# Performance work log

Measured on AMD Instinct MI355X. Metric: run time of the kernel, lower is better.

The kernel has to match this reference:

```python
import jax, jax.numpy as jnp
import numpy as np

DIM = 3
N = DIM * DIM          # 9 digits
NUM_NODES = N * N      # 81 cells
HID = 96
EMB = 16

def sudoku_edges():
    edges = []
    for r in range(N):
        for c in range(N):
            s = set()
            for k in range(N):
                s.add(r * N + k)
                s.add(k * N + c)
            br, bc = (r // DIM) * DIM, (c // DIM) * DIM
            for dr in range(DIM):
                for dc in range(DIM):
                    s.add((br + dr) * N + (bc + dc))
            s.discard(r * N + c)
            edges.append(sorted(s))
    return np.asarray(edges, np.int32)  # (81, 20)

EDGES = jnp.asarray(sudoku_edges())

def mlp(x, params):
    # ReLU between hidden layers, no activation after the last layer
    for w, b in params[:-1]:
        x = jax.nn.relu(x @ w + b)
    w, b = params[-1]
    return x @ w + b

def setup_inputs():
    key = jax.random.key(0)
    ks = iter(jax.random.split(key, 64))
    B = 256
    def p(shape, scale=0.1):
        return jax.random.normal(next(ks), shape, jnp.float32) * scale
    inp = {}
    inp['grids'] = jax.random.randint(next(ks), (B, NUM_NODES), 0, 3)
    inp['iters'] = 8
    inp['emb'] = p((3, EMB))
    inp['in_w0'] = p((EMB, HID)); inp['in_b0'] = jnp.zeros((HID,), jnp.float32)
    inp['in_w1'] = p((HID, HID)); inp['in_b1'] = jnp.zeros((HID,), jnp.float32)
    inp['in_w2'] = p((HID, HID)); inp['in_b2'] = jnp.zeros((HID,), jnp.float32)
    inp['rel_w0'] = p((2 * HID, HID)); inp['rel_b0'] = jnp.zeros((HID,), jnp.float32)
    inp['rel_w1'] = p((HID, HID)); inp['rel_b1'] = jnp.zeros((HID,), jnp.float32)
    inp['rel_w2'] = p((HID, HID)); inp['rel_b2'] = jnp.zeros((HID,), jnp.float32)
    inp['g_w0'] = p((2 * HID, HID)); inp['g_b0'] = jnp.zeros((HID,), jnp.float32)
    inp['g_w1'] = p((HID, HID)); inp['g_b1'] = jnp.zeros((HID,), jnp.float32)
    inp['g_w2'] = p((HID, HID)); inp['g_b2'] = jnp.zeros((HID,), jnp.float32)
    inp['lstm_wih'] = p((HID, 4 * HID)); inp['lstm_whh'] = p((HID, 4 * HID))
    inp['lstm_bih'] = jnp.zeros((4 * HID,), jnp.float32)
    inp['lstm_bhh'] = jnp.zeros((4 * HID,), jnp.float32)
    inp['r_w0'] = p((HID, HID)); inp['r_b0'] = jnp.zeros((HID,), jnp.float32)
    inp['r_w1'] = p((HID, HID)); inp['r_b1'] = jnp.zeros((HID,), jnp.float32)
    inp['r_w2'] = p((HID, N)); inp['r_b2'] = jnp.zeros((N,), jnp.float32)
    inp['c0'] = p((B * NUM_NODES, HID), 1.0)  # torch.randn LSTM cell init
    return inp

def reference(grids, iters, emb, in_w0, in_b0, in_w1, in_b1, in_w2, in_b2,
              rel_w0, rel_b0, rel_w1, rel_b1, rel_w2, rel_b2,
              g_w0, g_b0, g_w1, g_b1, g_w2, g_b2,
              lstm_wih, lstm_whh, lstm_bih, lstm_bhh,
              r_w0, r_b0, r_w1, r_b1, r_w2, r_b2, c0):
    B = grids.shape[0]
    in_p = [(in_w0, in_b0), (in_w1, in_b1), (in_w2, in_b2)]
    rel_p = [(rel_w0, rel_b0), (rel_w1, rel_b1), (rel_w2, rel_b2)]
    g_p = [(g_w0, g_b0), (g_w1, g_b1), (g_w2, g_b2)]
    r_p = [(r_w0, r_b0), (r_w1, r_b1), (r_w2, r_b2)]
    X = mlp(emb[grids], in_p)                     # (B, 81, 96)
    H0 = jax.lax.stop_gradient(X)                 # X.clone().detach()
    h = H0.reshape(B * NUM_NODES, HID)
    bias = lstm_bih + lstm_bhh

    def step(carry, _):
        h, c = carry
        Hn = h.reshape(B, NUM_NODES, HID)
        nbr = Hn[:, EDGES]                        # (B, 81, 20, 96) neighbor gather
        self_f = jnp.broadcast_to(Hn[:, :, None], nbr.shape)
        msgs = mlp(jnp.concatenate([self_f, nbr], axis=-1), rel_p)
        M = msgs.sum(axis=2)                      # scatter-sum of messages
        x_in = mlp(jnp.concatenate([X, M], axis=-1), g_p).reshape(B * NUM_NODES, HID)
        gates = x_in @ lstm_wih + h @ lstm_whh + bias
        i, f, g, o = jnp.split(gates, 4, axis=-1)  # torch gate order i,f,g,o
        c2 = jax.nn.sigmoid(f) * c + jax.nn.sigmoid(i) * jnp.tanh(g)
        h2 = jax.nn.sigmoid(o) * jnp.tanh(c2)
        out = mlp(h2.reshape(B, NUM_NODES, HID), r_p)  # (B, 81, 9)
        return (h2, c2), out

    _, outputs = jax.lax.scan(step, (h, c0), None, length=iters)
    return outputs  # (iters, B, 81, 9)
```

## Files before the change

### kernel.cpp

```cpp
#include <hip/hip_runtime.h>
#include <hip/hip_bf16.h>
#include <stdint.h>

typedef __attribute__((ext_vector_type(8))) short short8v;
typedef __attribute__((ext_vector_type(4))) float float4v;

#define DEVI __device__ __forceinline__

constexpr int BATCH = 256;
constexpr int NN   = 81;
constexpr int HID  = 96;
constexpr int NOUT = 9;
constexpr int BLOCK = 512;
constexpr int LDA = 100;
constexpr int LDB = 104;

constexpr int OFF_XG = 0;
constexpr int OFF_H0 = 7776;
constexpr int OFF_H1 = 11988;
constexpr int OFF_MS = 16200;
constexpr int OFF_AP = 24300;
constexpr int OFF_BV = 32400;
constexpr int SMEM_F = 40500;

constexpr int W_REL0A = 0;
constexpr int W_REL0B = 18432;
constexpr int W_REL1  = 36864;
constexpr int W_REL2  = 55296;
constexpr int W_G0B   = 73728;
constexpr int W_G1    = 92160;
constexpr int W_G2    = 110592;
constexpr int W_IH    = 129024;
constexpr int W_HH    = 202752;
constexpr int W_R0    = 276480;
constexpr int W_R1    = 294912;
constexpr int W_R2    = 313344;
constexpr int W_IN1   = 316416;
constexpr int W_IN2   = 334848;
constexpr int W_G0A   = 353280;

DEVI float sigm(float x)  { return 1.f / (1.f + __expf(-x)); }
DEVI float tanh_(float x) { return 1.f - 2.f / (__expf(2.f * x) + 1.f); }

DEVI short bfhi(float x) { union { float f; unsigned u; } v; v.f = x; return (short)(v.u >> 16); }
DEVI float fromBits(short s) { union { unsigned u; float f; } v; v.u = ((unsigned)(unsigned short)s) << 16; return v.f; }
DEVI short bfrne(float x) {
  union { float f; unsigned u; } v; v.f = x;
  unsigned r = v.u + 0x7fffu + ((v.u >> 16) & 1u);
  return (short)(r >> 16);
}
DEVI void split1(float x, short& h, short& l) { h = bfhi(x); l = bfrne(x - fromBits(h)); }

DEVI void packFrag(const float* p, short8v& v) {
  const float4 a = *reinterpret_cast<const float4*>(p);
  const float4 b = *reinterpret_cast<const float4*>(p + 4);
  v[0] = bfrne(a.x); v[1] = bfrne(a.y); v[2] = bfrne(a.z); v[3] = bfrne(a.w);
  v[4] = bfrne(b.x); v[5] = bfrne(b.y); v[6] = bfrne(b.z); v[7] = bfrne(b.w);
}
DEVI void packFragPair(const float* ap, const float* bp, short8v& v) {
  const float4 a0 = *reinterpret_cast<const float4*>(ap);
  const float4 a1 = *reinterpret_cast<const float4*>(ap + 4);
  const float4 b0 = *reinterpret_cast<const float4*>(bp);
  const float4 b1 = *reinterpret_cast<const float4*>(bp + 4);
  v[0] = bfrne(fmaxf(a0.x + b0.x, 0.f)); v[1] = bfrne(fmaxf(a0.y + b0.y, 0.f));
  v[2] = bfrne(fmaxf(a0.z + b0.z, 0.f)); v[3] = bfrne(fmaxf(a0.w + b0.w, 0.f));
  v[4] = bfrne(fmaxf(a1.x + b1.x, 0.f)); v[5] = bfrne(fmaxf(a1.y + b1.y, 0.f));
  v[6] = bfrne(fmaxf(a1.z + b1.z, 0.f)); v[7] = bfrne(fmaxf(a1.w + b1.w, 0.f));
}

DEVI float4v mfma2(short8v a, short8v bh, short8v bl, float4v acc) {
  acc = __builtin_amdgcn_mfma_f32_16x16x32_bf16(a, bh, acc, 0, 0, 0);
  acc = __builtin_amdgcn_mfma_f32_16x16x32_bf16(a, bl, acc, 0, 0, 0);
  return acc;
}

DEVI int nbr_of(int n, int e) {
  const int r = n / 9, c = n - 9 * r;
  if (e < 8)  { int cc = c + 1 + e;  if (cc >= 9) cc -= 9; return r * 9 + cc; }
  if (e < 16) { int rr = r + e - 7;  if (rr >= 9) rr -= 9; return rr * 9 + c; }
  const int q = e - 16, dr = 1 + (q >> 1), dc = 1 + (q & 1);
  const int rm = r % 3, cm = c % 3;
  int rr = r - rm + rm + dr; rr -= (rm + dr >= 3) ? 3 : 0;
  int cc = c - cm + cm + dc; cc -= (cm + dc >= 3) ? 3 : 0;
  return rr * 9 + cc;
}

__global__ __launch_bounds__(64)
void pack_kernel(const float* rel_w0, const float* rel_w1, const float* rel_w2,
                 const float* g_w0, const float* g_w1, const float* g_w2,
                 const float* wih, const float* whh,
                 const float* r_w0, const float* r_w1, const float* r_w2,
                 const float* in_w1, const float* in_w2, short* ws)
{
  const int lane = threadIdx.x;
  const int blk = blockIdx.x;
  const int starts[16] = {0,18,36,54,72,90,108,126,198,270,288,306,309,327,345,363};
  int mi = 0;
  while (blk >= starts[mi + 1]) ++mi;
  const int tt = blk - starts[mi];
  const int ntile = starts[mi + 1] - starts[mi];
  const float* src; int C = 96, row0 = 0, off;
  switch (mi) {
    case 0:  src = rel_w0; off = W_REL0A; break;
    case 1:  src = rel_w0; row0 = 96; off = W_REL0B; break;
    case 2:  src = rel_w1; off = W_REL1; break;
    case 3:  src = rel_w2; off = W_REL2; break;
    case 4:  src = g_w0; row0 = 96; off = W_G0B; break;
    case 5:  src = g_w1; off = W_G1; break;
    case 6:  src = g_w2; off = W_G2; break;
    case 7:  src = wih; C = 384; off = W_IH; break;
    case 8:  src = whh; C = 384; off = W_HH; break;
    case 9:  src = r_w0; off = W_R0; break;
    case 10: src = r_w1; off = W_R1; break;
    case 11: src = r_w2; C = 9; off = W_R2; break;
    case 12: src = in_w1; off = W_IN1; break;
    case 13: src = in_w2; off = W_IN2; break;
    default: src = g_w0; off = W_G0A; break;
  }
  const int kt = tt % 3, ct = tt / 3;
  const int q = lane >> 4, r = lane & 15;
  const int c = ct * 16 + r;
  short* hd = ws + off + tt * 512 + lane * 8;
  short* ld = hd + ntile * 512;
  #pragma unroll
  for (int j = 0; j < 8; ++j) {
    const int k = row0 + kt * 32 + q * 8 + j;
    float w = (c < C) ? src[k * C + c] : 0.f;
    short h, l; split1(w, h, l);
    hd[j] = h; ld[j] = l;
  }
}

template<bool ABF, bool OBF, bool RELU, bool XGADD>
DEVI void stage96(float* sm, int aOff, const short* WS, int wOff, int wTiles,
                  const float* bias, float bscale, int dOff, int dstLDf,
                  int wave, int lane)
{
  const int rl = lane & 15, q = lane >> 4;
  const int plane = wTiles * 512;
  const short* asb = reinterpret_cast<const short*>(sm + aOff);
  short* dsb = reinterpret_cast<short*>(sm + dOff);
  float* dsf = sm + dOff;
  #pragma unroll 1
  for (int t = wave; t < 18; t += 8) {
    const int rtp = t % 3, ct = t / 3;
    short8v a2[2][3];
    #pragma unroll
    for (int sub = 0; sub < 2; ++sub) {
      const int row = rtp * 32 + sub * 16 + rl;
      if (ABF) {
        const short* ap = asb + row * LDB + q * 8;
        #pragma unroll
        for (int kt = 0; kt < 3; ++kt)
          a2[sub][kt] = *reinterpret_cast<const short8v*>(ap + kt * 32);
      } else {
        const float* ap = &sm[aOff + row * LDA + q * 8];
        #pragma unroll
        for (int kt = 0; kt < 3; ++kt) packFrag(ap + kt * 32, a2[sub][kt]);
      }
    }
    float4v acc0 = {0.f, 0.f, 0.f, 0.f}, acc1 = {0.f, 0.f, 0.f, 0.f};
    #pragma unroll
    for (int kt = 0; kt < 3; ++kt) {
      const short* bp = WS + wOff + (ct * 3 + kt) * 512 + lane * 8;
      const short8v bh = *reinterpret_cast<const short8v*>(bp);
      const short8v bl = *reinterpret_cast<const short8v*>(bp + plane);
      acc0 = mfma2(a2[0][kt], bh, bl, acc0);
      acc1 = mfma2(a2[1][kt], bh, bl, acc1);
    }
    const int col = ct * 16 + rl;
    #pragma unroll
    for (int sub = 0; sub < 2; ++sub) {
      #pragma unroll
      for (int j = 0; j < 4; ++j) {
        const int row = rtp * 32 + sub * 16 + q * 4 + j;
        if (row < NN) {
          float v = sub ? acc1[j] : acc0[j];
          if (bias)  v += bias[col] * bscale;
          if (XGADD) v += sm[OFF_XG + row * 96 + col];
          if (RELU)  v = fmaxf(v, 0.f);
          if (OBF) dsb[row * LDB + col] = bfrne(v);
          else     dsf[row * dstLDf + col] = v;
        }
      }
    }
  }
}

__global__ __launch_bounds__(BLOCK) __attribute__((amdgpu_waves_per_eu(1, 2)))
void rrn_kernel(const int* __restrict__ grids, const int* __restrict__ itersp,
                const float* __restrict__ emb, const float* __restrict__ in_w0,
                const float* __restrict__ in_b0, const float* __restrict__ in_b1,
                const float* __restrict__ in_b2,
                const float* __restrict__ rel_b0, const float* __restrict__ rel_b1,
                const float* __restrict__ rel_b2,
                const float* __restrict__ g_b0, const float* __restrict__ g_b1,
                const float* __restrict__ g_b2,
                const float* __restrict__ bih, const float* __restrict__ bhh,
                const float* __restrict__ r_b0, const float* __restrict__ r_b1,
                const float* __restrict__ r_b2,
                const float* __restrict__ c0, const short* __restrict__ WS,
                float* __restrict__ out)
{
  __shared__ float sm[SMEM_F];
  const int b = blockIdx.x, tid = threadIdx.x;
  const int wave = tid >> 6, lane = tid & 63;
  const int rl = lane & 15, q = lane >> 4;
  const int iters = itersp[0];

  float creg[6][4];
  #pragma unroll
  for (int rt = 0; rt < 6; ++rt)
    #pragma unroll
    for (int j = 0; j < 4; ++j) creg[rt][j] = 0.f;
  if (wave < 6) {
    #pragma unroll
    for (int rt = 0; rt < 6; ++rt) {
      #pragma unroll
      for (int j = 0; j < 4; ++j) {
        const int n = rt * 16 + q * 4 + j, col = wave * 16 + rl;
        creg[rt][j] = (n < NN) ? c0[(size_t)b * NN * HID + n * HID + col] : 0.f;
      }
    }
  }

  for (int t = tid; t < NN * HID; t += BLOCK) {
    const int n = t / HID, col = t - n * HID;
    const int g = grids[b * NN + n];
    float acc = in_b0[col];
    #pragma unroll
    for (int k = 0; k < 16; ++k) acc += emb[g * 16 + k] * in_w0[k * HID + col];
    sm[OFF_AP + n * LDA + col] = fmaxf(acc, 0.f);
  }
  __syncthreads();
  stage96<false, true, true,  false>(sm, OFF_AP, WS, W_IN1, 18, in_b1, 1.f, OFF_MS, 0, wave, lane);
  __syncthreads();
  stage96<true,  true, false, false>(sm, OFF_MS, WS, W_IN2, 18, in_b2, 1.f, OFF_H0, 0, wave, lane);
  __syncthreads();
  stage96<true, false, false, false>(sm, OFF_H0, WS, W_G0A, 18, g_b0,  1.f, OFF_XG, 96, wave, lane);
  __syncthreads();

  for (int it = 0; it < iters; ++it) {
    const int hc = (it & 1) ? OFF_H1 : OFF_H0;
    const int hn = (it & 1) ? OFF_H0 : OFF_H1;

    for (int i = tid; i < 8100; i += BLOCK) sm[OFF_MS + i] = 0.f;
    stage96<true, false, false, false>(sm, hc, WS, W_REL0A, 18, rel_b0, 1.f, OFF_AP, LDA, wave, lane);
    stage96<true, false, false, false>(sm, hc, WS, W_REL0B, 18, nullptr, 0.f, OFF_BV, LDA, wave, lane);
    __syncthreads();

    #pragma unroll 1
    for (int g2 = wave; g2 < 51; g2 += 8) {
      short8v a2[2][3];
      #pragma unroll
      for (int sub = 0; sub < 2; ++sub) {
        const int row = g2 * 32 + sub * 16 + rl;
        if (row < 1620) {
          const int n = row / 20, e = row - 20 * n, m = nbr_of(n, e);
          const float* ap = &sm[OFF_AP + n * LDA + q * 8];
          const float* bp = &sm[OFF_BV + m * LDA + q * 8];
          #pragma unroll
          for (int kt = 0; kt < 3; ++kt)
            packFragPair(ap + kt * 32, bp + kt * 32, a2[sub][kt]);
        } else {
          const short8v z = {0,0,0,0,0,0,0,0};
          #pragma unroll
          for (int kt = 0; kt < 3; ++kt) a2[sub][kt] = z;
        }
      }
      #pragma unroll 1
      for (int ct = 0; ct < 6; ++ct) {
        const float rb1c = rel_b1[ct * 16 + rl];
        float4v acc0 = {0,0,0,0}, acc1 = {0,0,0,0};
        #pragma unroll
        for (int kt = 0; kt < 3; ++kt) {
          const short* bp = WS + W_REL1 + (ct * 3 + kt) * 512 + lane * 8;
          const short8v bh = *reinterpret_cast<const short8v*>(bp);
          const short8v bl = *reinterpret_cast<const short8v*>(bp + 18 * 512);
          acc0 = mfma2(a2[0][kt], bh, bl, acc0);
          acc1 = mfma2(a2[1][kt], bh, bl, acc1);
        }
        const int col = ct * 16 + rl;
        #pragma unroll
        for (int sub = 0; sub < 2; ++sub) {
          const int r0 = g2 * 32 + sub * 16 + q * 4;
          if (r0 < 1620) {
            const int node = r0 / 20;
            const float4v a = sub ? acc1 : acc0;
            const float s = fmaxf(a[0] + rb1c, 0.f) + fmaxf(a[1] + rb1c, 0.f)
                          + fmaxf(a[2] + rb1c, 0.f) + fmaxf(a[3] + rb1c, 0.f);
            atomicAdd(&sm[OFF_MS + node * LDA + col], s);
          }
        }
        __builtin_amdgcn_sched_barrier(0);
      }
    }
    __syncthreads();

    stage96<false, true, false, false>(sm, OFF_MS, WS, W_REL2, 18, rel_b2, 20.f, OFF_AP, 0, wave, lane);
    __syncthreads();
    stage96<true, true, true, true >(sm, OFF_AP, WS, W_G0B, 18, nullptr, 0.f, OFF_MS, 0, wave, lane);
    __syncthreads();
    stage96<true, true, true, false>(sm, OFF_MS, WS, W_G1, 18, g_b1, 1.f, OFF_AP, 0, wave, lane);
    __syncthreads();
    stage96<true, true, false, false>(sm, OFF_AP, WS, W_G2, 18, g_b2, 1.f, OFF_MS, 0, wave, lane);
    __syncthreads();

    if (wave < 6) {
      const int colh = wave * 16 + rl;
      const short* xs = reinterpret_cast<const short*>(sm + OFF_MS);
      const short* hs = reinterpret_cast<const short*>(sm + hc);
      short* hnp = reinterpret_cast<short*>(sm + hn);
      #pragma unroll
      for (int rt = 0; rt < 6; ++rt) {
        const int row = rt * 16 + rl;
        short8v af[6];
        #pragma unroll
        for (int kt = 0; kt < 3; ++kt)
          af[kt] = *reinterpret_cast<const short8v*>(xs + row * LDB + kt * 32 + q * 8);
        #pragma unroll
        for (int kt = 3; kt < 6; ++kt)
          af[kt] = *reinterpret_cast<const short8v*>(hs + row * LDB + (kt - 3) * 32 + q * 8);
        float4v ga[4];
        #pragma unroll
        for (int gate = 0; gate < 4; ++gate) {
          const int ct = gate * 6 + wave;
          float4v acc = {0.f, 0.f, 0.f, 0.f};
          #pragma unroll
          for (int kt = 0; kt < 3; ++kt) {
            const short* bp = WS + W_IH + (ct * 3 + kt) * 512 + lane * 8;
            acc = mfma2(af[kt], *reinterpret_cast<const short8v*>(bp),
                        *reinterpret_cast<const short8v*>(bp + 72 * 512), acc);
          }
          __builtin_amdgcn_sched_barrier(0);
          #pragma unroll
          for (int kt = 3; kt < 6; ++kt) {
            const short* bp = WS + W_HH + (ct * 3 + kt - 3) * 512 + lane * 8;
            acc = mfma2(af[kt], *reinterpret_cast<const short8v*>(bp),
                        *reinterpret_cast<const short8v*>(bp + 72 * 512), acc);
          }
          ga[gate] = acc;
          __builtin_amdgcn_sched_barrier(0);
        }
        #pragma unroll
        for (int j = 0; j < 4; ++j) {
          const int n = rt * 16 + q * 4 + j;
          const float gi = ga[0][j] + bih[colh]       + bhh[colh];
          const float gf = ga[1][j] + bih[96 + colh]  + bhh[96 + colh];
          const float gg = ga[2][j] + bih[192 + colh] + bhh[192 + colh];
          const float go = ga[3][j] + bih[288 + colh] + bhh[288 + colh];
          const float c2 = sigm(gf) * creg[rt][j] + sigm(gi) * tanh_(gg);
          creg[rt][j] = c2;
          if (n < NN) hnp[n * LDB + colh] = bfrne(sigm(go) * tanh_(c2));
        }
      }
    }
    __syncthreads();

    stage96<true, true, true, false>(sm, hn, WS, W_R0, 18, r_b0, 1.f, OFF_AP, 0, wave, lane);
    __syncthreads();
    stage96<true, true, true, false>(sm, OFF_AP, WS, W_R1, 18, r_b1, 1.f, OFF_MS, 0, wave, lane);
    __syncthreads();
    if (wave < 3) {
      const int rtp = wave;
      const short* asb = reinterpret_cast<const short*>(sm + OFF_MS);
      short8v a2[2][3];
      #pragma unroll
      for (int sub = 0; sub < 2; ++sub) {
        const int row = rtp * 32 + sub * 16 + rl;
        #pragma unroll
        for (int kt = 0; kt < 3; ++kt)
          a2[sub][kt] = *reinterpret_cast<const short8v*>(asb + row * LDB + kt * 32 + q * 8);
      }
      float4v a0 = {0,0,0,0}, a1 = {0,0,0,0};
      #pragma unroll
      for (int kt = 0; kt < 3; ++kt) {
        const short* bp = WS + W_R2 + kt * 512 + lane * 8;
        const short8v bh = *reinterpret_cast<const short8v*>(bp);
        const short8v bl = *reinterpret_cast<const short8v*>(bp + 3 * 512);
        a0 = mfma2(a2[0][kt], bh, bl, a0);
        a1 = mfma2(a2[1][kt], bh, bl, a1);
      }
      if (rl < NOUT) {
        float* op = out + ((size_t)it * BATCH + b) * NN * NOUT;
        #pragma unroll
        for (int sub = 0; sub < 2; ++sub)
          #pragma unroll
          for (int j = 0; j < 4; ++j) {
            const int row = rtp * 32 + sub * 16 + q * 4 + j;
            if (row < NN) op[row * NOUT + rl] = (sub ? a1[j] : a0[j]) + r_b2[rl];
          }
      }
    }
    __syncthreads();
  }
}

extern "C" void kernel_launch(void* const* d_in, const int* in_sizes, int n_in,
                              void* d_out, int out_size, void* d_ws, size_t ws_size,
                              hipStream_t stream) {
  (void)in_sizes; (void)n_in; (void)out_size; (void)ws_size;
  const int* grids = (const int*)d_in[0];
  const int* iters = (const int*)d_in[1];
  const float *emb = (const float*)d_in[2],
    *in_w0 = (const float*)d_in[3],  *in_b0 = (const float*)d_in[4],
    *in_b1 = (const float*)d_in[6],  *in_b2 = (const float*)d_in[8],
    *rel_w0 = (const float*)d_in[9],  *rel_b0 = (const float*)d_in[10],
    *rel_w1 = (const float*)d_in[11], *rel_b1 = (const float*)d_in[12],
    *rel_w2 = (const float*)d_in[13], *rel_b2 = (const float*)d_in[14],
    *g_w0 = (const float*)d_in[15], *g_b0 = (const float*)d_in[16],
    *g_w1 = (const float*)d_in[17], *g_b1 = (const float*)d_in[18],
    *g_w2 = (const float*)d_in[19], *g_b2 = (const float*)d_in[20],
    *wih = (const float*)d_in[21], *whh = (const float*)d_in[22],
    *bih = (const float*)d_in[23], *bhh = (const float*)d_in[24],
    *r_w0 = (const float*)d_in[25], *r_b0 = (const float*)d_in[26],
    *r_w1 = (const float*)d_in[27], *r_b1 = (const float*)d_in[28],
    *r_w2 = (const float*)d_in[29], *r_b2 = (const float*)d_in[30],
    *c0 = (const float*)d_in[31];
  short* ws = (short*)d_ws;
  pack_kernel<<<dim3(363), dim3(64), 0, stream>>>(
      rel_w0, rel_w1, rel_w2, g_w0, g_w1, g_w2, wih, whh,
      r_w0, r_w1, r_w2, (const float*)d_in[5], (const float*)d_in[7], ws);
  rrn_kernel<<<dim3(BATCH), dim3(BLOCK), 0, stream>>>(
      grids, iters, emb, in_w0, in_b0, in_b1, in_b2,
      rel_b0, rel_b1, rel_b2, g_b0, g_b1, g_b2,
      bih, bhh, r_b0, r_b1, r_b2, c0, (const short*)ws, (float*)d_out);
}
```

Before: 823.4 us.

## Double block to 16 waves and split all stages into finer per-wave tiles

New measurement: 1.204 ms. 1.46x slower.

```diff
diff --git a/kernel.cpp b/kernel.cpp
--- a/kernel.cpp
+++ b/kernel.cpp
@@ -11,7 +11,8 @@
 constexpr int NN   = 81;
 constexpr int HID  = 96;
 constexpr int NOUT = 9;
-constexpr int BLOCK = 512;
+constexpr int BLOCK = 1024;
+constexpr int NW   = 16;
 constexpr int LDA = 100;
 constexpr int LDB = 104;
 
@@ -142,52 +143,44 @@
   short* dsb = reinterpret_cast<short*>(sm + dOff);
   float* dsf = sm + dOff;
   #pragma unroll 1
-  for (int t = wave; t < 18; t += 8) {
-    const int rtp = t % 3, ct = t / 3;
-    short8v a2[2][3];
-    #pragma unroll
-    for (int sub = 0; sub < 2; ++sub) {
-      const int row = rtp * 32 + sub * 16 + rl;
-      if (ABF) {
-        const short* ap = asb + row * LDB + q * 8;
-        #pragma unroll
-        for (int kt = 0; kt < 3; ++kt)
-          a2[sub][kt] = *reinterpret_cast<const short8v*>(ap + kt * 32);
-      } else {
-        const float* ap = &sm[aOff + row * LDA + q * 8];
-        #pragma unroll
-        for (int kt = 0; kt < 3; ++kt) packFrag(ap + kt * 32, a2[sub][kt]);
-      }
-    }
-    float4v acc0 = {0.f, 0.f, 0.f, 0.f}, acc1 = {0.f, 0.f, 0.f, 0.f};
+  for (int t = wave; t < 36; t += NW) {
+    const int rt = t % 6, ct = t / 6;
+    const int row = rt * 16 + rl;
+    short8v a2[3];
+    if (ABF) {
+      const short* ap = asb + row * LDB + q * 8;
+      #pragma unroll
+      for (int kt = 0; kt < 3; ++kt)
+        a2[kt] = *reinterpret_cast<const short8v*>(ap + kt * 32);
+    } else {
+      const float* ap = &sm[aOff + row * LDA + q * 8];
+      #pragma unroll
+      for (int kt = 0; kt < 3; ++kt) packFrag(ap + kt * 32, a2[kt]);
+    }
+    float4v acc = {0.f, 0.f, 0.f, 0.f};
     #pragma unroll
     for (int kt = 0; kt < 3; ++kt) {
       const short* bp = WS + wOff + (ct * 3 + kt) * 512 + lane * 8;
-      const short8v bh = *reinterpret_cast<const short8v*>(bp);
-      const short8v bl = *reinterpret_cast<const short8v*>(bp + plane);
-      acc0 = mfma2(a2[0][kt], bh, bl, acc0);
-      acc1 = mfma2(a2[1][kt], bh, bl, acc1);
+      acc = mfma2(a2[kt], *reinterpret_cast<const short8v*>(bp),
+                  *reinterpret_cast<const short8v*>(bp + plane), acc);
     }
     const int col = ct * 16 + rl;
     #pragma unroll
-    for (int sub = 0; sub < 2; ++sub) {
-      #pragma unroll
-      for (int j = 0; j < 4; ++j) {
-        const int row = rtp * 32 + sub * 16 + q * 4 + j;
-        if (row < NN) {
-          float v = sub ? acc1[j] : acc0[j];
-          if (bias)  v += bias[col] * bscale;
-          if (XGADD) v += sm[OFF_XG + row * 96 + col];
-          if (RELU)  v = fmaxf(v, 0.f);
-          if (OBF) dsb[row * LDB + col] = bfrne(v);
-          else     dsf[row * dstLDf + col] = v;
-        }
-      }
-    }
-  }
-}
-
-__global__ __launch_bounds__(BLOCK) __attribute__((amdgpu_waves_per_eu(1, 2)))
+    for (int j = 0; j < 4; ++j) {
+      const int r2 = rt * 16 + q * 4 + j;
+      if (r2 < NN) {
+        float v = acc[j];
+        if (bias)  v += bias[col] * bscale;
+        if (XGADD) v += sm[OFF_XG + r2 * 96 + col];
+        if (RELU)  v = fmaxf(v, 0.f);
+        if (OBF) dsb[r2 * LDB + col] = bfrne(v);
+        else     dsf[r2 * dstLDf + col] = v;
+      }
+    }
+  }
+}
+
+__global__ __launch_bounds__(BLOCK)
 void rrn_kernel(const int* __restrict__ grids, const int* __restrict__ itersp,
                 const float* __restrict__ emb, const float* __restrict__ in_w0,
                 const float* __restrict__ in_b0, const float* __restrict__ in_b1,
@@ -208,18 +201,19 @@
   const int rl = lane & 15, q = lane >> 4;
   const int iters = itersp[0];
 
-  float creg[6][4];
+  const int cc7 = wave >> 1, half7 = wave & 1;
+  float creg[3][4];
   #pragma unroll
-  for (int rt = 0; rt < 6; ++rt)
+  for (int r3 = 0; r3 < 3; ++r3)
     #pragma unroll
-    for (int j = 0; j < 4; ++j) creg[rt][j] = 0.f;
-  if (wave < 6) {
+    for (int j = 0; j < 4; ++j) creg[r3][j] = 0.f;
+  if (wave < 12) {
     #pragma unroll
-    for (int rt = 0; rt < 6; ++rt) {
+    for (int r3 = 0; r3 < 3; ++r3) {
       #pragma unroll
       for (int j = 0; j < 4; ++j) {
-        const int n = rt * 16 + q * 4 + j, col = wave * 16 + rl;
-        creg[rt][j] = (n < NN) ? c0[(size_t)b * NN * HID + n * HID + col] : 0.f;
+        const int n = (half7 * 3 + r3) * 16 + q * 4 + j, col = cc7 * 16 + rl;
+        creg[r3][j] = (n < NN) ? c0[(size_t)b * NN * HID + n * HID + col] : 0.f;
       }
     }
   }
@@ -250,7 +244,7 @@
     __syncthreads();
 
     #pragma unroll 1
-    for (int g2 = wave; g2 < 51; g2 += 8) {
+    for (int g2 = wave; g2 < 51; g2 += NW) {
       short8v a2[2][3];
       #pragma unroll
       for (int sub = 0; sub < 2; ++sub) {
@@ -306,13 +300,14 @@
     stage96<true, true, false, false>(sm, OFF_AP, WS, W_G2, 18, g_b2, 1.f, OFF_MS, 0, wave, lane);
     __syncthreads();
 
-    if (wave < 6) {
-      const int colh = wave * 16 + rl;
+    if (wave < 12) {
+      const int colh = cc7 * 16 + rl;
       const short* xs = reinterpret_cast<const short*>(sm + OFF_MS);
       const short* hs = reinterpret_cast<const short*>(sm + hc);
       short* hnp = reinterpret_cast<short*>(sm + hn);
       #pragma unroll
-      for (int rt = 0; rt < 6; ++rt) {
+      for (int r3 = 0; r3 < 3; ++r3) {
+        const int rt = half7 * 3 + r3;
         const int row = rt * 16 + rl;
         short8v af[6];
         #pragma unroll
@@ -324,7 +319,7 @@
         float4v ga[4];
         #pragma unroll
         for (int gate = 0; gate < 4; ++gate) {
-          const int ct = gate * 6 + wave;
+          const int ct = gate * 6 + cc7;
           float4v acc = {0.f, 0.f, 0.f, 0.f};
           #pragma unroll
           for (int kt = 0; kt < 3; ++kt) {
@@ -349,8 +344,8 @@
           const float gf = ga[1][j] + bih[96 + colh]  + bhh[96 + colh];
           const float gg = ga[2][j] + bih[192 + colh] + bhh[192 + colh];
           const float go = ga[3][j] + bih[288 + colh] + bhh[288 + colh];
-          const float c2 = sigm(gf) * creg[rt][j] + sigm(gi) * tanh_(gg);
-          creg[rt][j] = c2;
+          const float c2 = sigm(gf) * creg[r3][j] + sigm(gi) * tanh_(gg);
+          creg[r3][j] = c2;
           if (n < NN) hnp[n * LDB + colh] = bfrne(sigm(go) * tanh_(c2));
         }
       }
@@ -361,35 +356,28 @@
     __syncthreads();
     stage96<true, true, true, false>(sm, OFF_AP, WS, W_R1, 18, r_b1, 1.f, OFF_MS, 0, wave, lane);
     __syncthreads();
-    if (wave < 3) {
-      const int rtp = wave;
+    if (wave < 6) {
+      const int rt6 = wave;
       const short* asb = reinterpret_cast<const short*>(sm + OFF_MS);
-      short8v a2[2][3];
-      #pragma unroll
-      for (int sub = 0; sub < 2; ++sub) {
-        const int row = rtp * 32 + sub * 16 + rl;
-        #pragma unroll
-        for (int kt = 0; kt < 3; ++kt)
-          a2[sub][kt] = *reinterpret_cast<const short8v*>(asb + row * LDB + kt * 32 + q * 8);
-      }
-      float4v a0 = {0,0,0,0}, a1 = {0,0,0,0};
+      const int row = rt6 * 16 + rl;
+      short8v a2[3];
+      #pragma unroll
+      for (int kt = 0; kt < 3; ++kt)
+        a2[kt] = *reinterpret_cast<const short8v*>(asb + row * LDB + kt * 32 + q * 8);
+      float4v acc = {0,0,0,0};
       #pragma unroll
       for (int kt = 0; kt < 3; ++kt) {
         const short* bp = WS + W_R2 + kt * 512 + lane * 8;
-        const short8v bh = *reinterpret_cast<const short8v*>(bp);
-        const short8v bl = *reinterpret_cast<const short8v*>(bp + 3 * 512);
-        a0 = mfma2(a2[0][kt], bh, bl, a0);
-        a1 = mfma2(a2[1][kt], bh, bl, a1);
+        acc = mfma2(a2[kt], *reinterpret_cast<const short8v*>(bp),
+                    *reinterpret_cast<const short8v*>(bp + 3 * 512), acc);
       }
       if (rl < NOUT) {
         float* op = out + ((size_t)it * BATCH + b) * NN * NOUT;
         #pragma unroll
-        for (int sub = 0; sub < 2; ++sub)
-          #pragma unroll
-          for (int j = 0; j < 4; ++j) {
-            const int row = rtp * 32 + sub * 16 + q * 4 + j;
-            if (row < NN) op[row * NOUT + rl] = (sub ? a1[j] : a0[j]) + r_b2[rl];
-          }
+        for (int j = 0; j < 4; ++j) {
+          const int r2 = rt6 * 16 + q * 4 + j;
+          if (r2 < NN) op[r2 * NOUT + rl] = acc[j] + r_b2[rl];
+        }
       }
     }
     __syncthreads();
```

## Retile message MLP to 16-row tiles, hoist LSTM biases, spread readout over six waves

Applied to the files above, without the earlier changes.

After: 1.087 ms. +32.0%, slower.

```diff
diff --git a/kernel.cpp b/kernel.cpp
--- a/kernel.cpp
+++ b/kernel.cpp
@@ -250,47 +250,49 @@
     __syncthreads();
 
     #pragma unroll 1
-    for (int g2 = wave; g2 < 51; g2 += 8) {
-      short8v a2[2][3];
-      #pragma unroll
-      for (int sub = 0; sub < 2; ++sub) {
-        const int row = g2 * 32 + sub * 16 + rl;
-        if (row < 1620) {
-          const int n = row / 20, e = row - 20 * n, m = nbr_of(n, e);
-          const float* ap = &sm[OFF_AP + n * LDA + q * 8];
-          const float* bp = &sm[OFF_BV + m * LDA + q * 8];
-          #pragma unroll
-          for (int kt = 0; kt < 3; ++kt)
-            packFragPair(ap + kt * 32, bp + kt * 32, a2[sub][kt]);
-        } else {
-          const short8v z = {0,0,0,0,0,0,0,0};
-          #pragma unroll
-          for (int kt = 0; kt < 3; ++kt) a2[sub][kt] = z;
-        }
+    for (int g1 = wave; g1 < 102; g1 += 8) {
+      const int base = g1 * 16;
+      const int row = base + rl;
+      short8v a2[3];
+      if (row < 1620) {
+        const int n = row / 20, e = row - 20 * n, m = nbr_of(n, e);
+        const float* ap = &sm[OFF_AP + n * LDA + q * 8];
+        const float* bp = &sm[OFF_BV + m * LDA + q * 8];
+        #pragma unroll
+        for (int kt = 0; kt < 3; ++kt)
+          packFragPair(ap + kt * 32, bp + kt * 32, a2[kt]);
+      } else {
+        const short8v z = {0,0,0,0,0,0,0,0};
+        #pragma unroll
+        for (int kt = 0; kt < 3; ++kt) a2[kt] = z;
       }
       #pragma unroll 1
-      for (int ct = 0; ct < 6; ++ct) {
-        const float rb1c = rel_b1[ct * 16 + rl];
-        float4v acc0 = {0,0,0,0}, acc1 = {0,0,0,0};
+      for (int cp = 0; cp < 3; ++cp) {
+        const int ctA = cp * 2, ctB = ctA + 1;
+        const float rbA = rel_b1[ctA * 16 + rl];
+        const float rbB = rel_b1[ctB * 16 + rl];
+        float4v accA = {0,0,0,0}, accB = {0,0,0,0};
         #pragma unroll
         for (int kt = 0; kt < 3; ++kt) {
-          const short* bp = WS + W_REL1 + (ct * 3 + kt) * 512 + lane * 8;
-          const short8v bh = *reinterpret_cast<const short8v*>(bp);
-          const short8v bl = *reinterpret_cast<const short8v*>(bp + 18 * 512);
-          acc0 = mfma2(a2[0][kt], bh, bl, acc0);
-          acc1 = mfma2(a2[1][kt], bh, bl, acc1);
-        }
-        const int col = ct * 16 + rl;
-        #pragma unroll
-        for (int sub = 0; sub < 2; ++sub) {
-          const int r0 = g2 * 32 + sub * 16 + q * 4;
-          if (r0 < 1620) {
-            const int node = r0 / 20;
-            const float4v a = sub ? acc1 : acc0;
-            const float s = fmaxf(a[0] + rb1c, 0.f) + fmaxf(a[1] + rb1c, 0.f)
-                          + fmaxf(a[2] + rb1c, 0.f) + fmaxf(a[3] + rb1c, 0.f);
-            atomicAdd(&sm[OFF_MS + node * LDA + col], s);
-          }
+          const short* bpA = WS + W_REL1 + (ctA * 3 + kt) * 512 + lane * 8;
+          accA = mfma2(a2[kt], *reinterpret_cast<const short8v*>(bpA),
+                       *reinterpret_cast<const short8v*>(bpA + 18 * 512), accA);
+        }
+        #pragma unroll
+        for (int kt = 0; kt < 3; ++kt) {
+          const short* bpB = WS + W_REL1 + (ctB * 3 + kt) * 512 + lane * 8;
+          accB = mfma2(a2[kt], *reinterpret_cast<const short8v*>(bpB),
+                       *reinterpret_cast<const short8v*>(bpB + 18 * 512), accB);
+        }
+        const int r0 = base + q * 4;
+        if (r0 < 1620) {
+          const int node = r0 / 20;
+          const float sA = fmaxf(accA[0] + rbA, 0.f) + fmaxf(accA[1] + rbA, 0.f)
+                         + fmaxf(accA[2] + rbA, 0.f) + fmaxf(accA[3] + rbA, 0.f);
+          const float sB = fmaxf(accB[0] + rbB, 0.f) + fmaxf(accB[1] + rbB, 0.f)
+                         + fmaxf(accB[2] + rbB, 0.f) + fmaxf(accB[3] + rbB, 0.f);
+          atomicAdd(&sm[OFF_MS + node * LDA + ctA * 16 + rl], sA);
+          atomicAdd(&sm[OFF_MS + node * LDA + ctB * 16 + rl], sB);
         }
         __builtin_amdgcn_sched_barrier(0);
       }
@@ -308,10 +310,14 @@
 
     if (wave < 6) {
       const int colh = wave * 16 + rl;
+      const float bI = bih[colh]       + bhh[colh];
+      const float bF = bih[96 + colh]  + bhh[96 + colh];
+      const float bG = bih[192 + colh] + bhh[192 + colh];
+      const float bO = bih[288 + colh] + bhh[288 + colh];
       const short* xs = reinterpret_cast<const short*>(sm + OFF_MS);
       const short* hs = reinterpret_cast<const short*>(sm + hc);
       short* hnp = reinterpret_cast<short*>(sm + hn);
-      #pragma unroll
+      #pragma unroll 1
       for (int rt = 0; rt < 6; ++rt) {
         const int row = rt * 16 + rl;
         short8v af[6];
@@ -332,7 +338,6 @@
             acc = mfma2(af[kt], *reinterpret_cast<const short8v*>(bp),
                         *reinterpret_cast<const short8v*>(bp + 72 * 512), acc);
           }
-          __builtin_amdgcn_sched_barrier(0);
           #pragma unroll
           for (int kt = 3; kt < 6; ++kt) {
             const short* bp = WS + W_HH + (ct * 3 + kt - 3) * 512 + lane * 8;
@@ -345,10 +350,10 @@
         #pragma unroll
         for (int j = 0; j < 4; ++j) {
           const int n = rt * 16 + q * 4 + j;
-          const float gi = ga[0][j] + bih[colh]       + bhh[colh];
-          const float gf = ga[1][j] + bih[96 + colh]  + bhh[96 + colh];
-          const float gg = ga[2][j] + bih[192 + colh] + bhh[192 + colh];
-          const float go = ga[3][j] + bih[288 + colh] + bhh[288 + colh];
+          const float gi = ga[0][j] + bI;
+          const float gf = ga[1][j] + bF;
+          const float gg = ga[2][j] + bG;
+          const float go = ga[3][j] + bO;
           const float c2 = sigm(gf) * creg[rt][j] + sigm(gi) * tanh_(gg);
           creg[rt][j] = c2;
           if (n < NN) hnp[n * LDB + colh] = bfrne(sigm(go) * tanh_(c2));
@@ -361,35 +366,28 @@
     __syncthreads();
     stage96<true, true, true, false>(sm, OFF_AP, WS, W_R1, 18, r_b1, 1.f, OFF_MS, 0, wave, lane);
     __syncthreads();
-    if (wave < 3) {
-      const int rtp = wave;
+    if (wave < 6) {
+      const int rt6 = wave;
       const short* asb = reinterpret_cast<const short*>(sm + OFF_MS);
-      short8v a2[2][3];
+      const int row = rt6 * 16 + rl;
+      short8v a2[3];
       #pragma unroll
-      for (int sub = 0; sub < 2; ++sub) {
-        const int row = rtp * 32 + sub * 16 + rl;
-        #pragma unroll
-        for (int kt = 0; kt < 3; ++kt)
-          a2[sub][kt] = *reinterpret_cast<const short8v*>(asb + row * LDB + kt * 32 + q * 8);
-      }
-      float4v a0 = {0,0,0,0}, a1 = {0,0,0,0};
+      for (int kt = 0; kt < 3; ++kt)
+        a2[kt] = *reinterpret_cast<const short8v*>(asb + row * LDB + kt * 32 + q * 8);
+      float4v acc = {0,0,0,0};
       #pragma unroll
       for (int kt = 0; kt < 3; ++kt) {
         const short* bp = WS + W_R2 + kt * 512 + lane * 8;
-        const short8v bh = *reinterpret_cast<const short8v*>(bp);
-        const short8v bl = *reinterpret_cast<const short8v*>(bp + 3 * 512);
-        a0 = mfma2(a2[0][kt], bh, bl, a0);
-        a1 = mfma2(a2[1][kt], bh, bl, a1);
+        acc = mfma2(a2[kt], *reinterpret_cast<const short8v*>(bp),
+                    *reinterpret_cast<const short8v*>(bp + 3 * 512), acc);
       }
       if (rl < NOUT) {
         float* op = out + ((size_t)it * BATCH + b) * NN * NOUT;
         #pragma unroll
-        for (int sub = 0; sub < 2; ++sub)
-          #pragma unroll
-          for (int j = 0; j < 4; ++j) {
-            const int row = rtp * 32 + sub * 16 + q * 4 + j;
-            if (row < NN) op[row * NOUT + rl] = (sub ? a1[j] : a0[j]) + r_b2[rl];
-          }
+        for (int j = 0; j < 4; ++j) {
+          const int r2 = rt6 * 16 + q * 4 + j;
+          if (r2 < NN) op[r2 * NOUT + rl] = acc[j] + r_b2[rl];
+        }
       }
     }
     __syncthreads();
```

## Fold linear layers rel_w2·g_w0B and g_w2·W_ih into combined weights

Applied to the files above, without the earlier changes.

Result: faster. 785.5 us (-4.6%).

```diff
diff --git a/kernel.cpp b/kernel.cpp
--- a/kernel.cpp
+++ b/kernel.cpp
@@ -26,18 +26,18 @@
 constexpr int W_REL0A = 0;
 constexpr int W_REL0B = 18432;
 constexpr int W_REL1  = 36864;
-constexpr int W_REL2  = 55296;
-constexpr int W_G0B   = 73728;
-constexpr int W_G1    = 92160;
-constexpr int W_G2    = 110592;
-constexpr int W_IH    = 129024;
-constexpr int W_HH    = 202752;
-constexpr int W_R0    = 276480;
-constexpr int W_R1    = 294912;
-constexpr int W_R2    = 313344;
-constexpr int W_IN1   = 316416;
-constexpr int W_IN2   = 334848;
-constexpr int W_G0A   = 353280;
+constexpr int W_COMB  = 55296;
+constexpr int W_G1    = 73728;
+constexpr int W_IHC   = 92160;
+constexpr int W_HH    = 165888;
+constexpr int W_R0    = 239616;
+constexpr int W_R1    = 258048;
+constexpr int W_R2    = 276480;
+constexpr int W_IN1   = 279552;
+constexpr int W_IN2   = 297984;
+constexpr int W_G0A   = 316416;
+constexpr int BC2OFF  = 334848;
+constexpr int B3OFF   = 335616;
 
 DEVI float sigm(float x)  { return 1.f / (1.f + __expf(-x)); }
 DEVI float tanh_(float x) { return 1.f - 2.f / (__expf(2.f * x) + 1.f); }
@@ -90,44 +90,73 @@
                  const float* g_w0, const float* g_w1, const float* g_w2,
                  const float* wih, const float* whh,
                  const float* r_w0, const float* r_w1, const float* r_w2,
-                 const float* in_w1, const float* in_w2, short* ws)
+                 const float* in_w1, const float* in_w2,
+                 const float* rel_b2, const float* g_b2, short* ws)
 {
   const int lane = threadIdx.x;
   const int blk = blockIdx.x;
-  const int starts[16] = {0,18,36,54,72,90,108,126,198,270,288,306,309,327,345,363};
+  if (blk == 327) {
+    float* bc2 = reinterpret_cast<float*>(ws + BC2OFF);
+    float* b3  = reinterpret_cast<float*>(ws + B3OFF);
+    for (int c = lane; c < 384; c += 64) {
+      float a = 0.f;
+      for (int t = 0; t < 96; ++t) a += g_b2[t] * wih[t * 384 + c];
+      bc2[c] = a;
+    }
+    for (int c = lane; c < 96; c += 64) {
+      float a = 0.f;
+      for (int t = 0; t < 96; ++t) a += 20.f * rel_b2[t] * g_w0[(96 + t) * 96 + c];
+      b3[c] = a;
+    }
+    return;
+  }
+  const int starts[14] = {0,18,36,54,72,90,162,234,252,270,273,291,309,327};
   int mi = 0;
   while (blk >= starts[mi + 1]) ++mi;
   const int tt = blk - starts[mi];
   const int ntile = starts[mi + 1] - starts[mi];
-  const float* src; int C = 96, row0 = 0, off;
+  const int kt = tt % 3, ct = tt / 3;
+  const int q = lane >> 4, r = lane & 15;
+  int off, C = 96, row0 = 0;
+  const float* src = nullptr;
   switch (mi) {
     case 0:  src = rel_w0; off = W_REL0A; break;
     case 1:  src = rel_w0; row0 = 96; off = W_REL0B; break;
     case 2:  src = rel_w1; off = W_REL1; break;
-    case 3:  src = rel_w2; off = W_REL2; break;
-    case 4:  src = g_w0; row0 = 96; off = W_G0B; break;
-    case 5:  src = g_w1; off = W_G1; break;
-    case 6:  src = g_w2; off = W_G2; break;
-    case 7:  src = wih; C = 384; off = W_IH; break;
-    case 8:  src = whh; C = 384; off = W_HH; break;
-    case 9:  src = r_w0; off = W_R0; break;
-    case 10: src = r_w1; off = W_R1; break;
-    case 11: src = r_w2; C = 9; off = W_R2; break;
-    case 12: src = in_w1; off = W_IN1; break;
-    case 13: src = in_w2; off = W_IN2; break;
+    case 3:  off = W_COMB; break;
+    case 4:  src = g_w1; off = W_G1; break;
+    case 5:  C = 384; off = W_IHC; break;
+    case 6:  src = whh; C = 384; off = W_HH; break;
+    case 7:  src = r_w0; off = W_R0; break;
+    case 8:  src = r_w1; off = W_R1; break;
+    case 9:  src = r_w2; C = 9; off = W_R2; break;
+    case 10: src = in_w1; off = W_IN1; break;
+    case 11: src = in_w2; off = W_IN2; break;
     default: src = g_w0; off = W_G0A; break;
   }
-  const int kt = tt % 3, ct = tt / 3;
-  const int q = lane >> 4, r = lane & 15;
   const int c = ct * 16 + r;
   short* hd = ws + off + tt * 512 + lane * 8;
   short* ld = hd + ntile * 512;
-  #pragma unroll
-  for (int j = 0; j < 8; ++j) {
-    const int k = row0 + kt * 32 + q * 8 + j;
-    float w = (c < C) ? src[k * C + c] : 0.f;
-    short h, l; split1(w, h, l);
-    hd[j] = h; ld[j] = l;
+  if (mi == 3 || mi == 5) {
+    const float* A  = (mi == 3) ? rel_w2 : g_w2;
+    const float* Bm = (mi == 3) ? (g_w0 + 96 * 96) : wih;
+    const int C2 = (mi == 3) ? 96 : 384;
+    float acc[8] = {0,0,0,0,0,0,0,0};
+    for (int t = 0; t < 96; ++t) {
+      const float bv = Bm[t * C2 + c];
+      #pragma unroll
+      for (int j = 0; j < 8; ++j) acc[j] += A[(kt * 32 + q * 8 + j) * 96 + t] * bv;
+    }
+    #pragma unroll
+    for (int j = 0; j < 8; ++j) { short h, l; split1(acc[j], h, l); hd[j] = h; ld[j] = l; }
+  } else {
+    #pragma unroll
+    for (int j = 0; j < 8; ++j) {
+      const int k = row0 + kt * 32 + q * 8 + j;
+      float w = (c < C) ? src[k * C + c] : 0.f;
+      short h, l; split1(w, h, l);
+      hd[j] = h; ld[j] = l;
+    }
   }
 }
 
@@ -193,9 +222,7 @@
                 const float* __restrict__ in_b0, const float* __restrict__ in_b1,
                 const float* __restrict__ in_b2,
                 const float* __restrict__ rel_b0, const float* __restrict__ rel_b1,
-                const float* __restrict__ rel_b2,
                 const float* __restrict__ g_b0, const float* __restrict__ g_b1,
-                const float* __restrict__ g_b2,
                 const float* __restrict__ bih, const float* __restrict__ bhh,
                 const float* __restrict__ r_b0, const float* __restrict__ r_b1,
                 const float* __restrict__ r_b2,
@@ -239,6 +266,9 @@
   __syncthreads();
   stage96<true, false, false, false>(sm, OFF_H0, WS, W_G0A, 18, g_b0,  1.f, OFF_XG, 96, wave, lane);
   __syncthreads();
+
+  const float* b3ptr = reinterpret_cast<const float*>(WS + B3OFF);
+  const float* bc2   = reinterpret_cast<const float*>(WS + BC2OFF);
 
   for (int it = 0; it < iters; ++it) {
     const int hc = (it & 1) ? OFF_H1 : OFF_H0;
@@ -297,17 +327,17 @@
     }
     __syncthreads();
 
-    stage96<false, true, false, false>(sm, OFF_MS, WS, W_REL2, 18, rel_b2, 20.f, OFF_AP, 0, wave, lane);
-    __syncthreads();
-    stage96<true, true, true, true >(sm, OFF_AP, WS, W_G0B, 18, nullptr, 0.f, OFF_MS, 0, wave, lane);
-    __syncthreads();
-    stage96<true, true, true, false>(sm, OFF_MS, WS, W_G1, 18, g_b1, 1.f, OFF_AP, 0, wave, lane);
-    __syncthreads();
-    stage96<true, true, false, false>(sm, OFF_AP, WS, W_G2, 18, g_b2, 1.f, OFF_MS, 0, wave, lane);
+    stage96<false, true, true, true>(sm, OFF_MS, WS, W_COMB, 18, b3ptr, 1.f, OFF_AP, 0, wave, lane);
+    __syncthreads();
+    stage96<true, true, true, false>(sm, OFF_AP, WS, W_G1, 18, g_b1, 1.f, OFF_MS, 0, wave, lane);
     __syncthreads();
 
     if (wave < 6) {
       const int colh = wave * 16 + rl;
+      const float bI = bih[colh]       + bhh[colh]       + bc2[colh];
+      const float bF = bih[96 + colh]  + bhh[96 + colh]  + bc2[96 + colh];
+      const float bG = bih[192 + colh] + bhh[192 + colh] + bc2[192 + colh];
+      const float bO = bih[288 + colh] + bhh[288 + colh] + bc2[288 + colh];
       const short* xs = reinterpret_cast<const short*>(sm + OFF_MS);
       const short* hs = reinterpret_cast<const short*>(sm + hc);
       short* hnp = reinterpret_cast<short*>(sm + hn);
@@ -328,7 +358,7 @@
           float4v acc = {0.f, 0.f, 0.f, 0.f};
           #pragma unroll
           for (int kt = 0; kt < 3; ++kt) {
-            const short* bp = WS + W_IH + (ct * 3 + kt) * 512 + lane * 8;
+            const short* bp = WS + W_IHC + (ct * 3 + kt) * 512 + lane * 8;
             acc = mfma2(af[kt], *reinterpret_cast<const short8v*>(bp),
                         *reinterpret_cast<const short8v*>(bp + 72 * 512), acc);
           }
@@ -345,10 +375,10 @@
         #pragma unroll
         for (int j = 0; j < 4; ++j) {
           const int n = rt * 16 + q * 4 + j;
-          const float gi = ga[0][j] + bih[colh]       + bhh[colh];
-          const float gf = ga[1][j] + bih[96 + colh]  + bhh[96 + colh];
-          const float gg = ga[2][j] + bih[192 + colh] + bhh[192 + colh];
-          const float go = ga[3][j] + bih[288 + colh] + bhh[288 + colh];
+          const float gi = ga[0][j] + bI;
+          const float gf = ga[1][j] + bF;
+          const float gg = ga[2][j] + bG;
+          const float go = ga[3][j] + bO;
           const float c2 = sigm(gf) * creg[rt][j] + sigm(gi) * tanh_(gg);
           creg[rt][j] = c2;
           if (n < NN) hnp[n * LDB + colh] = bfrne(sigm(go) * tanh_(c2));
@@ -361,35 +391,28 @@
     __syncthreads();
     stage96<true, true, true, false>(sm, OFF_AP, WS, W_R1, 18, r_b1, 1.f, OFF_MS, 0, wave, lane);
     __syncthreads();
-    if (wave < 3) {
-      const int rtp = wave;
+    if (wave < 6) {
+      const int rt6 = wave;
       const short* asb = reinterpret_cast<const short*>(sm + OFF_MS);
-      short8v a2[2][3];
-      #pragma unroll
-      for (int sub = 0; sub < 2; ++sub) {
-        const int row = rtp * 32 + sub * 16 + rl;
-        #pragma unroll
-        for (int kt = 0; kt < 3; ++kt)
-          a2[sub][kt] = *reinterpret_cast<const short8v*>(asb + row * LDB + kt * 32 + q * 8);
-      }
-      float4v a0 = {0,0,0,0}, a1 = {0,0,0,0};
+      const int row = rt6 * 16 + rl;
+      short8v a2[3];
+      #pragma unroll
+      for (int kt = 0; kt < 3; ++kt)
+        a2[kt] = *reinterpret_cast<const short8v*>(asb + row * LDB + kt * 32 + q * 8);
+      float4v acc = {0,0,0,0};
       #pragma unroll
       for (int kt = 0; kt < 3; ++kt) {
         const short* bp = WS + W_R2 + kt * 512 + lane * 8;
-        const short8v bh = *reinterpret_cast<const short8v*>(bp);
-        const short8v bl = *reinterpret_cast<const short8v*>(bp + 3 * 512);
-        a0 = mfma2(a2[0][kt], bh, bl, a0);
-        a1 = mfma2(a2[1][kt], bh, bl, a1);
+        acc = mfma2(a2[kt], *reinterpret_cast<const short8v*>(bp),
+                    *reinterpret_cast<const short8v*>(bp + 3 * 512), acc);
       }
       if (rl < NOUT) {
         float* op = out + ((size_t)it * BATCH + b) * NN * NOUT;
         #pragma unroll
-        for (int sub = 0; sub < 2; ++sub)
-          #pragma unroll
-          for (int j = 0; j < 4; ++j) {
-            const int row = rtp * 32 + sub * 16 + q * 4 + j;
-            if (row < NN) op[row * NOUT + rl] = (sub ? a1[j] : a0[j]) + r_b2[rl];
-          }
+        for (int j = 0; j < 4; ++j) {
+          const int r2 = rt6 * 16 + q * 4 + j;
+          if (r2 < NN) op[r2 * NOUT + rl] = acc[j] + r_b2[rl];
+        }
       }
     }
     __syncthreads();
@@ -404,7 +427,8 @@
   const int* iters = (const int*)d_in[1];
   const float *emb = (const float*)d_in[2],
     *in_w0 = (const float*)d_in[3],  *in_b0 = (const float*)d_in[4],
-    *in_b1 = (const float*)d_in[6],  *in_b2 = (const float*)d_in[8],
+    *in_w1 = (const float*)d_in[5],  *in_b1 = (const float*)d_in[6],
+    *in_w2 = (const float*)d_in[7],  *in_b2 = (const float*)d_in[8],
     *rel_w0 = (const float*)d_in[9],  *rel_b0 = (const float*)d_in[10],
     *rel_w1 = (const float*)d_in[11], *rel_b1 = (const float*)d_in[12],
     *rel_w2 = (const float*)d_in[13], *rel_b2 = (const float*)d_in[14],
@@ -418,11 +442,11 @@
     *r_w2 = (const float*)d_in[29], *r_b2 = (const float*)d_in[30],
     *c0 = (const float*)d_in[31];
   short* ws = (short*)d_ws;
-  pack_kernel<<<dim3(363), dim3(64), 0, stream>>>(
+  pack_kernel<<<dim3(328), dim3(64), 0, stream>>>(
       rel_w0, rel_w1, rel_w2, g_w0, g_w1, g_w2, wih, whh,
-      r_w0, r_w1, r_w2, (const float*)d_in[5], (const float*)d_in[7], ws);
+      r_w0, r_w1, r_w2, in_w1, in_w2, rel_b2, g_b2, ws);
   rrn_kernel<<<dim3(BATCH), dim3(BLOCK), 0, stream>>>(
       grids, iters, emb, in_w0, in_b0, in_b1, in_b2,
-      rel_b0, rel_b1, rel_b2, g_b0, g_b1, g_b2,
+      rel_b0, rel_b1, g_b0, g_b1,
       bih, bhh, r_b0, r_b1, r_b2, c0, (const short*)ws, (float*)d_out);
 }
```
